# Optimization experiments

Measured on AMD Instinct MI355X. Metric: run time of the kernel, lower is better.

## Reference

```python
import jax, jax.numpy as jnp
import numpy as np

EPS = 1e-6


def setup_inputs() -> dict:
    key = jax.random.key(0)
    k1, k2, k3, k4, k5, k6 = jax.random.split(key, 6)
    B, S = 32, 1024
    H, W = 32, 32            # max_n_patches_h/w
    C, P = 3, 16             # channels, patch_res
    D = C * P * P            # 768
    P2 = P * P               # 256
    patches = jax.random.normal(k1, (B, S, D), dtype=jnp.float32)
    pos_h = jax.random.randint(k2, (B, S), 0, H)
    pos_w = jax.random.randint(k3, (B, S), 0, W)
    key_pad_mask = jax.random.bernoulli(k4, 0.1, (B, S))  # True where padding
    n = jnp.zeros((H, W), dtype=jnp.float32)
    mean = 0.1 * jax.random.normal(k5, (H, W, P2), dtype=jnp.float32)
    m2 = jax.random.uniform(k6, (H, W, P2), dtype=jnp.float32)
    return {"patches": patches, "pos_h": pos_h, "pos_w": pos_w,
            "key_pad_mask": key_pad_mask, "n": n, "mean": mean, "m2": m2}


def reference(patches, pos_h, pos_w, key_pad_mask, n, mean, m2):
    """PatchNorm.forward in training mode (Welford update + normalize).

    Masked (padded) positions contribute 0 to the scatter sums and are
    written back as zeros, matching the torch boolean-mask gather/scatter.
    """
    H, W, P2 = mean.shape
    B, S, D = patches.shape
    C = D // P2
    HW = H * W

    x = patches.reshape(B * S, C, P2)                    # (N, c, p^2)
    pf = (pos_h * W + pos_w).reshape(-1)                 # (N,) flat grid index
    w = (~key_pad_mask).reshape(-1).astype(patches.dtype)  # 1.0 on valid tokens

    # --- Welford online update (torch scatter_add semantics w/ duplicates) ---
    counts = jax.ops.segment_sum(w, pf, num_segments=HW)
    n_new = n + counts.reshape(H, W)

    mean_flat = mean.reshape(HW, P2)
    delta = (x - mean_flat[pf][:, None, :]).mean(axis=1) * w[:, None]  # (N, p^2)
    n_g = jnp.maximum(n_new.reshape(HW)[pf], 1.0)
    mean_new_flat = mean_flat + jax.ops.segment_sum(delta / n_g[:, None], pf, num_segments=HW)
    mean_new = mean_new_flat.reshape(H, W, P2)

    delta2 = (x - mean_new_flat[pf][:, None, :]).mean(axis=1) * w[:, None]
    m2_new = m2 + jax.ops.segment_sum(delta * delta2, pf, num_segments=HW).reshape(H, W, P2)

    # --- var / std (var := 1 where n < 2) ---
    var = jnp.where((n_new < 2.0)[..., None], 1.0,
                    m2_new / jnp.maximum(n_new, 1.0)[..., None])
    std = jnp.sqrt(var)

    # --- normalize with gathered per-position stats, zero out padding ---
    mg = mean_new.reshape(HW, P2)[pf][:, None, :]        # (N, 1, p^2)
    sg = std.reshape(HW, P2)[pf][:, None, :]
    out = (x - mg) / (sg + EPS) * w[:, None, None]
    return out.reshape(B, S, D)
```

## Files before the change

kernel.cpp:

```cpp
#include <hip/hip_runtime.h>
#include <math.h>


#define EPSF 1e-6f

typedef float v4 __attribute__((ext_vector_type(4)));

static constexpr int W_GRID  = 32;
static constexpr int P2      = 256;
static constexpr int P4      = 64;
static constexpr int D4      = 192;
static constexpr int HW      = 1024;
static constexpr int NTOK    = 32768;
static constexpr int LISTCAP = 96;
static constexpr int SLICE   = NTOK / HW;

__global__ void k_pf(const int* __restrict__ pos_h,
                     const int* __restrict__ pos_w,
                     const int* __restrict__ mask,
                     unsigned short* __restrict__ pf16) {
    int i = blockIdx.x * blockDim.x + threadIdx.x;
    if (i >= NTOK) return;
    const int valid = (mask[i] == 0);
    pf16[i] = valid ? (unsigned short)(pos_h[i] * W_GRID + pos_w[i])
                    : (unsigned short)0xFFFF;
}

__global__ void __launch_bounds__(256, 4)
k_cell(const v4* __restrict__ patches4,
       const unsigned short* __restrict__ pf16,
       const float* __restrict__ n_old,
       const float* __restrict__ mean_old,
       const float* __restrict__ m2_old,
       v4* __restrict__ out4) {
    const int g    = blockIdx.x;
    const int tid  = threadIdx.x;
    const int wave = tid >> 6;
    const int lane = tid & 63;

    __shared__ int            list[LISTCAP];
    __shared__ int            s_cnt;
    __shared__ unsigned short s_slice[SLICE];
    __shared__ v4             l14[4][64];
    __shared__ v4             l24[4][64];
    __shared__ v4             mn_s[P4];
    __shared__ v4             is_s[P4];

    if (tid == 0) s_cnt = 0;
    if (tid < SLICE) s_slice[tid] = pf16[g * SLICE + tid];

    const int4* pp = (const int4*)pf16;
    int4 v[16];
#pragma unroll
    for (int it = 0; it < 16; ++it) v[it] = pp[it * 256 + tid];

    __syncthreads();

    const v4 zero4 = {0.f, 0.f, 0.f, 0.f};
#pragma unroll
    for (int t = 0; t < SLICE; ++t) {
        if (s_slice[t] == 0xFFFF) {
            const int i = g * SLICE + t;
            if (tid < D4)
                __builtin_nontemporal_store(zero4, out4 + (size_t)i * D4 + tid);
        }
    }

#pragma unroll
    for (int it = 0; it < 16; ++it) {
        const int base = (it * 256 + tid) * 8;
#pragma unroll
        for (int k = 0; k < 4; ++k) {
            const int word = (&v[it].x)[k];
            const int g0 = word & 0xFFFF;
            const int g1 = (word >> 16) & 0xFFFF;
            if (g0 == g) { int s = atomicAdd(&s_cnt, 1); if (s < LISTCAP) list[s] = base + 2 * k; }
            if (g1 == g) { int s = atomicAdd(&s_cnt, 1); if (s < LISTCAP) list[s] = base + 2 * k + 1; }
        }
    }
    __syncthreads();
    const int c = min(s_cnt, LISTCAP);

    v4 s1 = zero4;
    v4 s2 = zero4;
    for (int k = wave; k < c; k += 16) {
        int   idx[4];
        float wf[4];
#pragma unroll
        for (int j = 0; j < 4; ++j) {
            const int  kk  = k + 4 * j;
            const bool val = (kk < c);
            wf[j]  = val ? 1.0f : 0.0f;
            idx[j] = list[val ? kk : k];
        }
        v4 A[4], B[4], Dd[4];
#pragma unroll
        for (int j = 0; j < 4; ++j) {
            const v4* tp = patches4 + (size_t)idx[j] * D4 + lane;
            A[j]  = tp[0];
            B[j]  = tp[P4];
            Dd[j] = tp[2 * P4];
        }
#pragma unroll
        for (int j = 0; j < 4; ++j) {
            const v4 xb = (A[j] + B[j] + Dd[j]) * ((1.0f / 3.0f) * wf[j]);
            s1 += xb;
            s2 += xb * xb;
        }
    }

    l14[wave][lane] = s1;
    l24[wave][lane] = s2;
    __syncthreads();

    {
        const float* l1f = (const float*)l14;
        const float* l2f = (const float*)l24;
        const float S1 = l1f[tid] + l1f[256 + tid] + l1f[512 + tid] + l1f[768 + tid];
        const float S2 = l2f[tid] + l2f[256 + tid] + l2f[512 + tid] + l2f[768 + tid];

        const float cnt = (float)c;
        const float nn  = n_old[g] + cnt;
        const float ng  = fmaxf(nn, 1.0f);
        const int   j   = g * P2 + tid;
        const float mo  = mean_old[j];
        const float mn  = mo + (S1 - cnt * mo) / ng;
        const float m2n = m2_old[j] + (S2 - (mo + mn) * S1 + cnt * mo * mn);
        const float var = (nn < 2.0f) ? 1.0f : (m2n / ng);
        ((float*)mn_s)[tid] = mn;
        ((float*)is_s)[tid] = 1.0f / (sqrtf(var) + EPSF);
    }
    __syncthreads();

    const v4 m4 = mn_s[lane];
    const v4 s4 = is_s[lane];
    for (int k = wave; k < c; k += 16) {
        int  idx[4];
        bool val[4];
#pragma unroll
        for (int j = 0; j < 4; ++j) {
            const int kk = k + 4 * j;
            val[j] = (kk < c);
            idx[j] = list[val[j] ? kk : k];
        }
        v4 X[12];
#pragma unroll
        for (int j = 0; j < 4; ++j) {
            const v4* tp = patches4 + (size_t)idx[j] * D4 + lane;
            X[3 * j]     = __builtin_nontemporal_load(tp);
            X[3 * j + 1] = __builtin_nontemporal_load(tp + P4);
            X[3 * j + 2] = __builtin_nontemporal_load(tp + 2 * P4);
        }
#pragma unroll
        for (int j = 0; j < 4; ++j) {
            if (val[j]) {
                v4* op = out4 + (size_t)idx[j] * D4 + lane;
                __builtin_nontemporal_store((X[3 * j]     - m4) * s4, op);
                __builtin_nontemporal_store((X[3 * j + 1] - m4) * s4, op + P4);
                __builtin_nontemporal_store((X[3 * j + 2] - m4) * s4, op + 2 * P4);
            }
        }
    }
}

extern "C" void kernel_launch(void* const* d_in, const int* in_sizes, int n_in,
                              void* d_out, int out_size, void* d_ws, size_t ws_size,
                              hipStream_t stream) {
    const v4*  patches4 = (const v4*)d_in[0];
    const int* pos_h    = (const int*)d_in[1];
    const int* pos_w    = (const int*)d_in[2];
    const int* mask     = (const int*)d_in[3];
    const float* n_old  = (const float*)d_in[4];
    const float* mean   = (const float*)d_in[5];
    const float* m2     = (const float*)d_in[6];
    v4* out4 = (v4*)d_out;

    unsigned short* pf16 = (unsigned short*)d_ws;

    k_pf<<<NTOK / 256, 256, 0, stream>>>(pos_h, pos_w, mask, pf16);
    k_cell<<<HW, 256, 0, stream>>>(patches4, pf16, n_old, mean, m2, out4);
}
```

Baseline: 57.08 us.

## Split each grid cell across two blocks with atomic partial sums and spin barrier

```diff
diff --git a/kernel.cpp b/kernel.cpp
--- a/kernel.cpp
+++ b/kernel.cpp
@@ -12,28 +12,40 @@
 static constexpr int D4      = 192;
 static constexpr int HW      = 1024;
 static constexpr int NTOK    = 32768;
-static constexpr int LISTCAP = 96;
-static constexpr int SLICE   = NTOK / HW;
+static constexpr int NBLK    = 2 * HW;
+static constexpr int LISTCAP = 64;
+static constexpr int SLICE   = NTOK / NBLK;
+static constexpr int ZERO_V4 = (2 * HW * P2 * 4 + 2 * HW * 4 + 15) / 16;
 
 __global__ void k_pf(const int* __restrict__ pos_h,
                      const int* __restrict__ pos_w,
                      const int* __restrict__ mask,
-                     unsigned short* __restrict__ pf16) {
-    int i = blockIdx.x * blockDim.x + threadIdx.x;
-    if (i >= NTOK) return;
-    const int valid = (mask[i] == 0);
-    pf16[i] = valid ? (unsigned short)(pos_h[i] * W_GRID + pos_w[i])
-                    : (unsigned short)0xFFFF;
+                     unsigned short* __restrict__ pf16,
+                     v4* __restrict__ zero_base) {
+    const int i = blockIdx.x * 256 + threadIdx.x;
+    if (i < NTOK) {
+        const int valid = (mask[i] == 0);
+        pf16[i] = valid ? (unsigned short)(pos_h[i] * W_GRID + pos_w[i])
+                        : (unsigned short)0xFFFF;
+    }
+    const v4 zz = {0.f, 0.f, 0.f, 0.f};
+    for (int q = i; q < ZERO_V4; q += NTOK) zero_base[q] = zz;
 }
 
-__global__ void __launch_bounds__(256, 4)
+__global__ void __launch_bounds__(256, 8)
 k_cell(const v4* __restrict__ patches4,
        const unsigned short* __restrict__ pf16,
        const float* __restrict__ n_old,
        const float* __restrict__ mean_old,
        const float* __restrict__ m2_old,
+       float* __restrict__ S1p,
+       float* __restrict__ S2p,
+       int* __restrict__ cntp,
+       int* __restrict__ arrive,
        v4* __restrict__ out4) {
-    const int g    = blockIdx.x;
+    const int b    = blockIdx.x;
+    const int g    = b >> 1;
+    const int h    = b & 1;
     const int tid  = threadIdx.x;
     const int wave = tid >> 6;
     const int lane = tid & 63;
@@ -47,7 +59,7 @@
     __shared__ v4             is_s[P4];
 
     if (tid == 0) s_cnt = 0;
-    if (tid < SLICE) s_slice[tid] = pf16[g * SLICE + tid];
+    if (tid < SLICE) s_slice[tid] = pf16[b * SLICE + tid];
 
     const int4* pp = (const int4*)pf16;
     int4 v[16];
@@ -60,7 +72,7 @@
 #pragma unroll
     for (int t = 0; t < SLICE; ++t) {
         if (s_slice[t] == 0xFFFF) {
-            const int i = g * SLICE + t;
+            const int i = b * SLICE + t;
             if (tid < D4)
                 __builtin_nontemporal_store(zero4, out4 + (size_t)i * D4 + tid);
         }
@@ -72,10 +84,11 @@
 #pragma unroll
         for (int k = 0; k < 4; ++k) {
             const int word = (&v[it].x)[k];
-            const int g0 = word & 0xFFFF;
-            const int g1 = (word >> 16) & 0xFFFF;
-            if (g0 == g) { int s = atomicAdd(&s_cnt, 1); if (s < LISTCAP) list[s] = base + 2 * k; }
-            if (g1 == g) { int s = atomicAdd(&s_cnt, 1); if (s < LISTCAP) list[s] = base + 2 * k + 1; }
+            const int gg = (h ? (word >> 16) : word) & 0xFFFF;
+            if (gg == g) {
+                int s = atomicAdd(&s_cnt, 1);
+                if (s < LISTCAP) list[s] = base + 2 * k + h;
+            }
         }
     }
     __syncthreads();
@@ -112,14 +125,32 @@
     l14[wave][lane] = s1;
     l24[wave][lane] = s2;
     __syncthreads();
-
     {
         const float* l1f = (const float*)l14;
         const float* l2f = (const float*)l24;
-        const float S1 = l1f[tid] + l1f[256 + tid] + l1f[512 + tid] + l1f[768 + tid];
-        const float S2 = l2f[tid] + l2f[256 + tid] + l2f[512 + tid] + l2f[768 + tid];
-
-        const float cnt = (float)c;
+        const float S1h = l1f[tid] + l1f[256 + tid] + l1f[512 + tid] + l1f[768 + tid];
+        const float S2h = l2f[tid] + l2f[256 + tid] + l2f[512 + tid] + l2f[768 + tid];
+        atomicAdd(&S1p[g * P2 + tid], S1h);
+        atomicAdd(&S2p[g * P2 + tid], S2h);
+    }
+    if (tid == 0) atomicAdd(&cntp[g], c);
+    __syncthreads();
+
+    if (tid == 0) {
+        atomicAdd(&arrive[g], 1);
+        while (__hip_atomic_load(&arrive[g], __ATOMIC_ACQUIRE,
+                                 __HIP_MEMORY_SCOPE_AGENT) < 2) { }
+    }
+    __syncthreads();
+
+    {
+        const float S1 = __hip_atomic_load(&S1p[g * P2 + tid], __ATOMIC_RELAXED,
+                                           __HIP_MEMORY_SCOPE_AGENT);
+        const float S2 = __hip_atomic_load(&S2p[g * P2 + tid], __ATOMIC_RELAXED,
+                                           __HIP_MEMORY_SCOPE_AGENT);
+        const int cnt_i = __hip_atomic_load(&cntp[g], __ATOMIC_RELAXED,
+                                            __HIP_MEMORY_SCOPE_AGENT);
+        const float cnt = (float)cnt_i;
         const float nn  = n_old[g] + cnt;
         const float ng  = fmaxf(nn, 1.0f);
         const int   j   = g * P2 + tid;
@@ -176,7 +207,12 @@
     v4* out4 = (v4*)d_out;
 
     unsigned short* pf16 = (unsigned short*)d_ws;
-
-    k_pf<<<NTOK / 256, 256, 0, stream>>>(pos_h, pos_w, mask, pf16);
-    k_cell<<<HW, 256, 0, stream>>>(patches4, pf16, n_old, mean, m2, out4);
+    float* S1p   = (float*)(pf16 + NTOK);
+    float* S2p   = S1p + (size_t)HW * P2;
+    int*   cntp  = (int*)(S2p + (size_t)HW * P2);
+    int*   arrive = cntp + HW;
+
+    k_pf<<<NTOK / 256, 256, 0, stream>>>(pos_h, pos_w, mask, pf16, (v4*)S1p);
+    k_cell<<<NBLK, 256, 0, stream>>>(patches4, pf16, n_old, mean, m2,
+                                     S1p, S2p, cntp, arrive, out4);
 }
```

New measurement: 88.01 us. 54.2% more time.
